# Performance work log

Measured on AMD Instinct MI355X. Metric: run time of the kernel, lower is better.

The kernel has to match this reference:

```python
import jax, jax.numpy as jnp
import numpy as np

D_MODEL = 1024
NUM_HEADS = 16
HEAD_DIM = D_MODEL // NUM_HEADS
LN_EPS = 1e-3  # keras LayerNormalization default epsilon


def setup_inputs() -> dict:
    key = jax.random.key(0)
    ks = jax.random.split(key, 10)
    B, T = 2, 2048
    s = 1.0 / np.sqrt(D_MODEL)
    return {
        "x": jax.random.normal(ks[0], (B, T, D_MODEL), dtype=jnp.float32),
        "Wq": jax.random.normal(ks[1], (D_MODEL, D_MODEL), dtype=jnp.float32) * s,
        "Wk": jax.random.normal(ks[2], (D_MODEL, D_MODEL), dtype=jnp.float32) * s,
        "Wv": jax.random.normal(ks[3], (D_MODEL, D_MODEL), dtype=jnp.float32) * s,
        "Wg": jax.random.normal(ks[4], (D_MODEL, D_MODEL), dtype=jnp.float32) * s,
        "bg": jnp.zeros((D_MODEL,), dtype=jnp.float32),
        "Wo": jax.random.normal(ks[5], (D_MODEL, D_MODEL), dtype=jnp.float32) * s,
        "bo": jnp.zeros((D_MODEL,), dtype=jnp.float32),
        "ln_gamma": jnp.ones((D_MODEL,), dtype=jnp.float32),
        "ln_beta": jnp.zeros((D_MODEL,), dtype=jnp.float32),
    }


def reference(x, Wq, Wk, Wv, Wg, bg, Wo, bo, ln_gamma, ln_beta):
    B, T, D = x.shape
    H, dh = NUM_HEADS, HEAD_DIM

    def split_heads(z):
        return z.reshape(B, T, H, dh).transpose(0, 2, 1, 3)  # [B,H,T,dh]

    Q = split_heads(x @ Wq)
    K = split_heads(x @ Wk)
    V = split_heads(x @ Wv)
    G = jax.nn.swish(x @ Wg + bg)  # [B,T,D]

    # Per-head causal decay mask D[h,m,n] = gamma_h^(m-n) for m>=n else 0
    idx = jnp.arange(T, dtype=jnp.float32)
    diff = idx[:, None] - idx[None, :]  # [T,T]
    causal = (diff >= 0).astype(jnp.float32)
    gammas = 1.0 - 2.0 ** (-5.0 - jnp.arange(H, dtype=jnp.float32))  # [H]
    Dmask = (gammas[:, None, None] ** jnp.maximum(diff, 0.0)) * causal  # [H,T,T]

    scale = float(dh) ** 0.5
    scores = jnp.einsum('bhtd,bhsd->bhts', Q, K) / scale  # [B,H,T,T]
    ret = jnp.einsum('bhts,bhsd->bhtd', scores * Dmask[None], V)  # [B,H,T,dh]
    ret = ret.transpose(0, 2, 1, 3).reshape(B, T, D)  # concat heads

    # LayerNorm (axis=-1, keras default eps=1e-3)
    mu = jnp.mean(ret, axis=-1, keepdims=True)
    var = jnp.mean(jnp.square(ret - mu), axis=-1, keepdims=True)
    ln = (ret - mu) / jnp.sqrt(var + LN_EPS) * ln_gamma + ln_beta

    return (ln * G) @ Wo + bo
```

## Files before the change

### kernel.cpp

```cpp
#include <hip/hip_runtime.h>

#define D_MODEL 1024
#define NHEADS  16
#define HDIM    64
#define BATCH   2
#define SEQ     2048
#define ROWS    (BATCH*SEQ)
#define CHUNK   128
#define NCHUNK  (SEQ/CHUNK)
#define LN_EPS  1e-3f

typedef unsigned short ushort_t;
typedef __attribute__((ext_vector_type(4))) float          f32x4;
typedef __attribute__((ext_vector_type(8))) short          s16x8;
typedef __attribute__((ext_vector_type(4))) unsigned short u16x4;
typedef __attribute__((ext_vector_type(8))) unsigned short u16x8;

__device__ __forceinline__ ushort_t f2b(float f) {
    union { float f; unsigned int u; } v; v.f = f;
    unsigned int r = v.u + 0x7fffu + ((v.u >> 16) & 1u);
    return (ushort_t)(r >> 16);
}
__device__ __forceinline__ float b2f(ushort_t b) {
    union { unsigned int u; float f; } v; v.u = ((unsigned int)b) << 16;
    return v.f;
}

__device__ __forceinline__ void async_load16(const ushort_t* g, ushort_t* l) {
    __builtin_amdgcn_global_load_lds(
        (const __attribute__((address_space(1))) unsigned int*)(g),
        (__attribute__((address_space(3))) unsigned int*)(l),
        16, 0, 0);
}

__global__ __launch_bounds__(256) void prep_kernel(
        const float* __restrict__ x,
        const float* __restrict__ Wq, const float* __restrict__ Wk,
        const float* __restrict__ Wv, const float* __restrict__ Wg,
        const float* __restrict__ Wo,
        ushort_t* __restrict__ xb, ushort_t* __restrict__ WcatT,
        ushort_t* __restrict__ WoT, float* __restrict__ rowstats) {
    __shared__ float tile[32][33];
    int bid = blockIdx.x, t = threadIdx.x;
    if (bid < 4096) {
        if (bid < 8)
            *(f32x4*)(rowstats + (bid * 256 + t) * 4) = (f32x4)0.0f;
        int idx = (bid * 256 + t) * 4;
        f32x4 v = *(const f32x4*)(x + idx);
        u16x4 o;
        o.x = f2b(v.x); o.y = f2b(v.y); o.z = f2b(v.z); o.w = f2b(v.w);
        *(u16x4*)(xb + idx) = o;
        return;
    }
    int zb = bid - 4096;
    int z = zb >> 10;
    int rem = zb & 1023;
    int bx = rem & 31, by = rem >> 5;
    const float* W = (z == 0) ? Wq : (z == 1) ? Wk : (z == 2) ? Wv : (z == 3) ? Wg : Wo;
    ushort_t* dst = (z < 4) ? (WcatT + (size_t)z * 1024 * 1024) : WoT;
    int n0 = bx * 32, k0 = by * 32;
    int tx = t & 31, ty = t >> 5;
#pragma unroll
    for (int i = 0; i < 4; i++) {
        int k = k0 + ty + i * 8;
        tile[ty + i * 8][tx] = W[(size_t)k * 1024 + n0 + tx];
    }
    __syncthreads();
#pragma unroll
    for (int i = 0; i < 4; i++) {
        int n = n0 + ty + i * 8;
        dst[(size_t)n * 1024 + k0 + tx] = f2b(tile[tx][ty + i * 8]);
    }
}

__global__ __launch_bounds__(256, 2) void gemm_kernel(
        const ushort_t* __restrict__ A, const ushort_t* __restrict__ BT,
        int K, int N, int mode, const float* __restrict__ bias,
        ushort_t* __restrict__ Yout, float* __restrict__ Fout) {
    extern __shared__ char smem[];
    ushort_t* As = (ushort_t*)smem;
    ushort_t* Bs = As + 128 * 64;
    int t = threadIdx.x;
    int row0 = blockIdx.y * 128, col0 = blockIdx.x * 128;
    int w = t >> 6, lane = t & 63;
    int wr = (w >> 1) * 64, wc = (w & 1) * 64;
    int qd = lane >> 4, ln = lane & 15;
    int lx = ln & 7;

    f32x4 acc[4][4];
#pragma unroll
    for (int i = 0; i < 4; i++)
#pragma unroll
        for (int j = 0; j < 4; j++) acc[i][j] = (f32x4)0.0f;

    for (int k0 = 0; k0 < K; k0 += 64) {
#pragma unroll
        for (int p = 0; p < 4; p++) {
            int g = p * 256 + t;
            int r = g >> 3;
            int kb = g & 7;
            int kbs = kb ^ (r & 7);
            async_load16(A + (size_t)(row0 + r) * K + k0 + kbs * 8, As + g * 8);
            async_load16(BT + (size_t)(col0 + r) * K + k0 + kbs * 8, Bs + g * 8);
        }
        __syncthreads();
#pragma unroll
        for (int kk = 0; kk < 64; kk += 32) {
            s16x8 af[4], bf[4];
            int kxa = ((kk >> 3) + qd) ^ lx;
#pragma unroll
            for (int i = 0; i < 4; i++)
                af[i] = *(const s16x8*)(As + (wr + i * 16 + ln) * 64 + kxa * 8);
#pragma unroll
            for (int j = 0; j < 4; j++)
                bf[j] = *(const s16x8*)(Bs + (wc + j * 16 + ln) * 64 + kxa * 8);
#pragma unroll
            for (int i = 0; i < 4; i++)
#pragma unroll
                for (int j = 0; j < 4; j++)
                    acc[i][j] = __builtin_amdgcn_mfma_f32_16x16x32_bf16(
                        af[i], bf[j], acc[i][j], 0, 0, 0);
        }
        __syncthreads();
    }

#pragma unroll
    for (int i = 0; i < 4; i++)
#pragma unroll
        for (int j = 0; j < 4; j++) {
            int n = col0 + wc + j * 16 + ln;
            int region = n >> 10;
#pragma unroll
            for (int r = 0; r < 4; r++) {
                int m = row0 + wr + i * 16 + qd * 4 + r;
                float v = acc[i][j][r];
                if (mode == 0) {
                    if (region == 0) v *= 0.125f;
                    else if (region == 3) {
                        v += bias[n & 1023];
                        v = v / (1.0f + __expf(-v));
                    }
                    Yout[(size_t)m * N + n] = f2b(v);
                } else {
                    Fout[(size_t)m * N + n] = v + bias[n];
                }
            }
        }
}

#define LDW 72
#define SJ 136
#define VT_LDW 136
#define CO_ELEMS (128*LDW*2 + 64*LDW*2 + 64*VT_LDW)
__global__ __launch_bounds__(256, 2) void retention_kernel(const ushort_t* __restrict__ Y,
                                                           ushort_t* __restrict__ ret,
                                                           float* __restrict__ rowstats) {
    extern __shared__ char smem[];
    ushort_t* Qs   = (ushort_t*)smem;
    ushort_t* Kc   = Qs + 128 * LDW;
    ushort_t* Sphi = Kc + 128 * LDW;
    ushort_t* Splo = Sphi + 64 * LDW;
    ushort_t* Vt   = Splo + 64 * LDW;
    ushort_t* Pl   = Qs;
    ushort_t* Ktd  = Qs;
    ushort_t* Vtd  = Ktd + 64 * SJ;

    int c_raw = blockIdx.x, h = blockIdx.y, b = blockIdx.z;
    int c = b ? (NCHUNK - 1 - c_raw) : c_raw;
    int t = threadIdx.x;
    float gamma = 1.0f - exp2f(-5.0f - (float)h);
    float l2g = log2f(gamma);
    float gC = exp2f(128.0f * l2g);
    int row0 = b * SEQ + c * CHUNK;
    int colK = D_MODEL + h * HDIM;

    int w = t >> 6, lane = t & 63;
    int wr = w * 16;
    int qd = lane >> 4, ln = lane & 15;
    int dgi = t & 7, jg = t >> 3;

    {
        u16x8 v8[4];
#pragma unroll
        for (int r = 0; r < 4; r++)
            v8[r] = *(const u16x8*)(Y + (size_t)(row0 + jg * 4 + r) * 4096
                                      + 2 * D_MODEL + h * HDIM + dgi * 8);
#pragma unroll
        for (int q = 0; q < 8; q++) {
            int qq = q ^ dgi;
            u16x4 pv;
#pragma unroll
            for (int r = 0; r < 4; r++) pv[r] = v8[r][qq];
            *(u16x4*)(Vt + (dgi * 8 + qq) * VT_LDW + jg * 4) = pv;
        }
    }

    float dec[4];
#pragma unroll
    for (int r = 0; r < 4; r++)
        dec[r] = exp2f((float)(127 - (jg * 4 + r)) * l2g);

    f32x4 Sreg[4];
#pragma unroll
    for (int nt = 0; nt < 4; nt++) Sreg[nt] = (f32x4)0.0f;

    u16x8 k8[4], v8[4];
    if (c > 0) {
        int prow0 = b * SEQ;
#pragma unroll
        for (int r = 0; r < 4; r++) {
            size_t src = (size_t)(prow0 + jg * 4 + r) * 4096 + colK + dgi * 8;
            k8[r] = *(const u16x8*)(Y + src);
            v8[r] = *(const u16x8*)(Y + src + D_MODEL);
        }
    }

    for (int cp = 0; cp < c; cp++) {
        __syncthreads();
#pragma unroll
        for (int q = 0; q < 8; q++) {
            int qq = q ^ dgi;
            u16x4 pk, pv;
#pragma unroll
            for (int r = 0; r < 4; r++) {
                pk[r] = f2b(b2f(k8[r][qq]) * dec[r]);
                pv[r] = v8[r][qq];
            }
            *(u16x4*)(Ktd + (dgi * 8 + qq) * SJ + jg * 4) = pk;
            *(u16x4*)(Vtd + (dgi * 8 + qq) * SJ + jg * 4) = pv;
        }
        __syncthreads();
        if (cp + 1 < c) {
            int prow0 = b * SEQ + (cp + 1) * CHUNK;
#pragma unroll
            for (int r = 0; r < 4; r++) {
                size_t src = (size_t)(prow0 + jg * 4 + r) * 4096 + colK + dgi * 8;
                k8[r] = *(const u16x8*)(Y + src);
                v8[r] = *(const u16x8*)(Y + src + D_MODEL);
            }
        }
        s16x8 af[4];
#pragma unroll
        for (int ks = 0; ks < 4; ks++)
            af[ks] = *(const s16x8*)(Vtd + (wr + ln) * SJ + ks * 32 + qd * 8);
#pragma unroll
        for (int nt = 0; nt < 4; nt++) {
            f32x4 a4 = (f32x4)0.0f;
#pragma unroll
            for (int ks = 0; ks < 4; ks++) {
                s16x8 bf = *(const s16x8*)(Ktd + (nt * 16 + ln) * SJ + ks * 32 + qd * 8);
                a4 = __builtin_amdgcn_mfma_f32_16x16x32_bf16(af[ks], bf, a4, 0, 0, 0);
            }
            Sreg[nt] = Sreg[nt] * gC + a4;
        }
    }
    __syncthreads();

#pragma unroll
    for (int nt = 0; nt < 4; nt++)
#pragma unroll
        for (int r = 0; r < 4; r++) {
            int d = wr + qd * 4 + r, e = nt * 16 + ln;
            float s = Sreg[nt][r];
            ushort_t hb = f2b(s);
            Sphi[d * LDW + e] = hb;
            Splo[d * LDW + e] = f2b(s - b2f(hb));
        }

    for (int g = t; g < 1024; g += 256) {
        int i = g >> 3, dg = (g & 7) * 8;
        size_t src = (size_t)(row0 + i) * 4096 + h * HDIM + dg;
        *(u16x8*)(Qs + i * LDW + dg) = *(const u16x8*)(Y + src);
        *(u16x8*)(Kc + i * LDW + dg) = *(const u16x8*)(Y + src + D_MODEL);
    }
    __syncthreads();

    int wr2 = w * 32;

    s16x8 aq[2][2];
#pragma unroll
    for (int mt = 0; mt < 2; mt++)
#pragma unroll
        for (int ks = 0; ks < 2; ks++)
            aq[mt][ks] = *(const s16x8*)(Qs + (wr2 + mt * 16 + ln) * LDW + ks * 32 + qd * 8);

    float prow[2][4], pcolm[8];
#pragma unroll
    for (int mt = 0; mt < 2; mt++)
#pragma unroll
        for (int r = 0; r < 4; r++)
            prow[mt][r] = exp2f((float)(wr2 + mt * 16 + qd * 4 + r + 1) * l2g);
#pragma unroll
    for (int nt = 0; nt < 8; nt++)
        pcolm[nt] = exp2f(-(float)(nt * 16 + ln + 1) * l2g);

    f32x4 out[2][4];
#pragma unroll
    for (int mt = 0; mt < 2; mt++)
#pragma unroll
        for (int dt = 0; dt < 4; dt++) out[mt][dt] = (f32x4)0.0f;
#pragma unroll
    for (int dt = 0; dt < 4; dt++)
#pragma unroll
        for (int ks = 0; ks < 2; ks++) {
            s16x8 bh_ = *(const s16x8*)(Sphi + (dt * 16 + ln) * LDW + ks * 32 + qd * 8);
            s16x8 bl_ = *(const s16x8*)(Splo + (dt * 16 + ln) * LDW + ks * 32 + qd * 8);
#pragma unroll
            for (int mt = 0; mt < 2; mt++) {
                out[mt][dt] = __builtin_amdgcn_mfma_f32_16x16x32_bf16(
                    aq[mt][ks], bh_, out[mt][dt], 0, 0, 0);
                out[mt][dt] = __builtin_amdgcn_mfma_f32_16x16x32_bf16(
                    aq[mt][ks], bl_, out[mt][dt], 0, 0, 0);
            }
        }
#pragma unroll
    for (int mt = 0; mt < 2; mt++)
#pragma unroll
        for (int dt = 0; dt < 4; dt++)
#pragma unroll
            for (int r = 0; r < 4; r++) out[mt][dt][r] *= prow[mt][r];

    f32x4 sc[2][8];
#pragma unroll
    for (int mt = 0; mt < 2; mt++)
#pragma unroll
        for (int nt = 0; nt < 8; nt++) sc[mt][nt] = (f32x4)0.0f;
#pragma unroll
    for (int nt = 0; nt < 8; nt++)
#pragma unroll
        for (int ks = 0; ks < 2; ks++) {
            s16x8 bk = *(const s16x8*)(Kc + (nt * 16 + ln) * LDW + ks * 32 + qd * 8);
#pragma unroll
            for (int mt = 0; mt < 2; mt++)
                sc[mt][nt] = __builtin_amdgcn_mfma_f32_16x16x32_bf16(
                    aq[mt][ks], bk, sc[mt][nt], 0, 0, 0);
        }
    __syncthreads();

#pragma unroll
    for (int mt = 0; mt < 2; mt++)
#pragma unroll
        for (int nt = 0; nt < 8; nt++) {
            int j = nt * 16 + ln;
#pragma unroll
            for (int r = 0; r < 4; r++) {
                int i = wr2 + mt * 16 + qd * 4 + r;
                float v = (j <= i) ? sc[mt][nt][r] * (prow[mt][r] * pcolm[nt]) : 0.0f;
                Pl[i * VT_LDW + j] = f2b(v);
            }
        }
    __syncthreads();

#pragma unroll
    for (int ks = 0; ks < 4; ks++) {
        s16x8 ap[2];
#pragma unroll
        for (int mt = 0; mt < 2; mt++)
            ap[mt] = *(const s16x8*)(Pl + (wr2 + mt * 16 + ln) * VT_LDW + ks * 32 + qd * 8);
#pragma unroll
        for (int dt = 0; dt < 4; dt++) {
            s16x8 bv = *(const s16x8*)(Vt + (dt * 16 + ln) * VT_LDW + ks * 32 + qd * 8);
#pragma unroll
            for (int mt = 0; mt < 2; mt++)
                out[mt][dt] = __builtin_amdgcn_mfma_f32_16x16x32_bf16(
                    ap[mt], bv, out[mt][dt], 0, 0, 0);
        }
    }

    float psum[2][4], psq[2][4];
#pragma unroll
    for (int mt = 0; mt < 2; mt++)
#pragma unroll
        for (int r = 0; r < 4; r++) { psum[mt][r] = 0.0f; psq[mt][r] = 0.0f; }
#pragma unroll
    for (int mt = 0; mt < 2; mt++)
#pragma unroll
        for (int dt = 0; dt < 4; dt++)
#pragma unroll
            for (int r = 0; r < 4; r++) {
                int i = wr2 + mt * 16 + qd * 4 + r;
                ushort_t hb = f2b(out[mt][dt][r]);
                ret[(size_t)(row0 + i) * D_MODEL + h * HDIM + dt * 16 + ln] = hb;
                float vr = b2f(hb);
                psum[mt][r] += vr;
                psq[mt][r]  += vr * vr;
            }
#pragma unroll
    for (int m = 1; m < 16; m <<= 1)
#pragma unroll
        for (int mt = 0; mt < 2; mt++)
#pragma unroll
            for (int r = 0; r < 4; r++) {
                psum[mt][r] += __shfl_xor(psum[mt][r], m);
                psq[mt][r]  += __shfl_xor(psq[mt][r], m);
            }
    if (ln == 0) {
#pragma unroll
        for (int mt = 0; mt < 2; mt++)
#pragma unroll
            for (int r = 0; r < 4; r++) {
                int i = row0 + wr2 + mt * 16 + qd * 4 + r;
                atomicAdd(rowstats + 2 * i,     psum[mt][r]);
                atomicAdd(rowstats + 2 * i + 1, psq[mt][r]);
            }
    }
}

__global__ __launch_bounds__(256) void ln_gate_kernel(const ushort_t* __restrict__ ret,
                                                      const ushort_t* __restrict__ Y,
                                                      const float* __restrict__ rowstats,
                                                      const float* __restrict__ lgam,
                                                      const float* __restrict__ lbet,
                                                      ushort_t* __restrict__ LNG) {
    int row = blockIdx.x, t = threadIdx.x;
    float s  = rowstats[2 * row];
    float sq = rowstats[2 * row + 1];
    float mu  = s * (1.0f / 1024.0f);
    float var = sq * (1.0f / 1024.0f) - mu * mu;
    float inv = rsqrtf(var + LN_EPS);
    int col = t * 4;
    u16x4 rv = *(const u16x4*)(ret + (size_t)row * D_MODEL + col);
    u16x4 ug = *(const u16x4*)(Y + (size_t)row * 4096 + 3 * D_MODEL + col);
    f32x4 ga = *(const f32x4*)(lgam + col);
    f32x4 gb = *(const f32x4*)(lbet + col);
    u16x4 o;
#pragma unroll
    for (int k = 0; k < 4; k++)
        o[k] = f2b(((b2f(rv[k]) - mu) * inv * ga[k] + gb[k]) * b2f(ug[k]));
    *(u16x4*)(LNG + (size_t)row * D_MODEL + col) = o;
}

extern "C" void kernel_launch(void* const* d_in, const int* in_sizes, int n_in,
                              void* d_out, int out_size, void* d_ws, size_t ws_size,
                              hipStream_t stream) {
    const float* x   = (const float*)d_in[0];
    const float* Wq  = (const float*)d_in[1];
    const float* Wk  = (const float*)d_in[2];
    const float* Wv  = (const float*)d_in[3];
    const float* Wg  = (const float*)d_in[4];
    const float* bg  = (const float*)d_in[5];
    const float* Wo  = (const float*)d_in[6];
    const float* bo  = (const float*)d_in[7];
    const float* lng = (const float*)d_in[8];
    const float* lnb = (const float*)d_in[9];
    float* out = (float*)d_out;

    char* ws = (char*)d_ws;
    ushort_t* xb    = (ushort_t*)(ws);
    ushort_t* WcatT = (ushort_t*)(ws + (8ull  << 20));
    ushort_t* WoT   = (ushort_t*)(ws + (16ull << 20));
    ushort_t* Yb    = (ushort_t*)(ws + (18ull << 20));
    float*    rstat = (float*)   (ws + (50ull << 20));
    ushort_t* retb  = (ushort_t*)(ws + (51ull << 20));
    ushort_t* LNGb  = (ushort_t*)(ws + (60ull << 20));

    const int GEMM_LDS = 2 * 128 * 64 * 2;
    const int CO_BYTES = CO_ELEMS * 2;

    hipFuncSetAttribute(reinterpret_cast<const void*>(gemm_kernel),
                        hipFuncAttributeMaxDynamicSharedMemorySize, GEMM_LDS);
    hipFuncSetAttribute(reinterpret_cast<const void*>(retention_kernel),
                        hipFuncAttributeMaxDynamicSharedMemorySize, CO_BYTES);

    prep_kernel<<<4096 + 5120, 256, 0, stream>>>(x, Wq, Wk, Wv, Wg, Wo,
                                                 xb, WcatT, WoT, rstat);

    gemm_kernel<<<dim3(32, 32), 256, GEMM_LDS, stream>>>(
        xb, WcatT, 1024, 4096, 0, bg, Yb, (float*)nullptr);

    retention_kernel<<<dim3(NCHUNK, NHEADS, BATCH), 256, CO_BYTES, stream>>>(
        Yb, retb, rstat);

    ln_gate_kernel<<<ROWS, 256, 0, stream>>>(retb, Yb, rstat, lng, lnb, LNGb);

    gemm_kernel<<<dim3(8, 32), 256, GEMM_LDS, stream>>>(
        LNGb, WoT, 1024, 1024, 1, bo, (ushort_t*)nullptr, out);
}
```

Before: 223.1 us.

## Precompute per-chunk KV states in separate kernel, accumulate in retention kernel

Moves the per-chunk decayed K^T V state computation into a new chunk_states_kernel that runs in parallel over all chunks and writes fp32 states to a workspace. The retention kernel then only combines prior chunk states with a decay-weighted sum read from global memory, instead of recomputing MFMAs over every prior chunk serially. This removes the O(c) serial MFMA and LDS-transpose loop and the load imbalance that the reversed-chunk ordering tried to offset. It costs an extra kernel launch and about 8MB of fp32 state traffic. The combine loop is still O(c) global reads per block.

```diff
diff --git a/kernel.cpp b/kernel.cpp
--- a/kernel.cpp
+++ b/kernel.cpp
@@ -148,11 +148,78 @@
         }
 }
 
+#define SJ 136
+__global__ __launch_bounds__(256) void chunk_states_kernel(const ushort_t* __restrict__ Y,
+                                                           float* __restrict__ Astate) {
+    __shared__ ushort_t Ktd[64 * SJ];
+    __shared__ ushort_t Vtd[64 * SJ];
+    int c = blockIdx.x, h = blockIdx.y, b = blockIdx.z;
+    int t = threadIdx.x;
+    float gamma = 1.0f - exp2f(-5.0f - (float)h);
+    float l2g = log2f(gamma);
+    int row0 = b * SEQ + c * CHUNK;
+    int colK = D_MODEL + h * HDIM;
+
+    {
+        int dgi = t & 7, jg = t >> 3;
+        u16x8 k8[4], v8[4];
+        float dec[4];
+#pragma unroll
+        for (int r = 0; r < 4; r++) {
+            int j = jg * 4 + r;
+            size_t src = (size_t)(row0 + j) * 4096 + colK + dgi * 8;
+            k8[r] = *(const u16x8*)(Y + src);
+            v8[r] = *(const u16x8*)(Y + src + D_MODEL);
+            dec[r] = exp2f((float)(127 - j) * l2g);
+        }
+#pragma unroll
+        for (int q = 0; q < 8; q++) {
+            int qq = q ^ dgi;
+            u16x4 pk, pv;
+#pragma unroll
+            for (int r = 0; r < 4; r++) {
+                pk[r] = f2b(b2f(k8[r][qq]) * dec[r]);
+                pv[r] = v8[r][qq];
+            }
+            *(u16x4*)(Ktd + (dgi * 8 + qq) * SJ + jg * 4) = pk;
+            *(u16x4*)(Vtd + (dgi * 8 + qq) * SJ + jg * 4) = pv;
+        }
+    }
+    __syncthreads();
+
+    int w = t >> 6, lane = t & 63;
+    int wr = w * 16;
+    int qd = lane >> 4, ln = lane & 15;
+
+    s16x8 af[4];
+#pragma unroll
+    for (int ks = 0; ks < 4; ks++)
+        af[ks] = *(const s16x8*)(Vtd + (wr + ln) * SJ + ks * 32 + qd * 8);
+
+    f32x4 acc[4];
+#pragma unroll
+    for (int nt = 0; nt < 4; nt++) {
+        acc[nt] = (f32x4)0.0f;
+#pragma unroll
+        for (int ks = 0; ks < 4; ks++) {
+            s16x8 bf = *(const s16x8*)(Ktd + (nt * 16 + ln) * SJ + ks * 32 + qd * 8);
+            acc[nt] = __builtin_amdgcn_mfma_f32_16x16x32_bf16(af[ks], bf, acc[nt], 0, 0, 0);
+        }
+    }
+
+    size_t base = ((size_t)((b * NHEADS + h) * NCHUNK + c)) * 4096;
+#pragma unroll
+    for (int nt = 0; nt < 4; nt++)
+#pragma unroll
+        for (int r = 0; r < 4; r++)
+            Astate[base + (size_t)(wr + qd * 4 + r) * 64 + nt * 16 + ln] = acc[nt][r];
+}
+
 #define LDW 72
-#define SJ 136
 #define VT_LDW 136
 #define CO_ELEMS (128*LDW*2 + 64*LDW*2 + 64*VT_LDW)
 __global__ __launch_bounds__(256, 2) void retention_kernel(const ushort_t* __restrict__ Y,
+                                                           const float* __restrict__ Astate,
                                                            ushort_t* __restrict__ ret,
                                                            float* __restrict__ rowstats) {
     extern __shared__ char smem[];
@@ -162,20 +229,15 @@
     ushort_t* Splo = Sphi + 64 * LDW;
     ushort_t* Vt   = Splo + 64 * LDW;
     ushort_t* Pl   = Qs;
-    ushort_t* Ktd  = Qs;
-    ushort_t* Vtd  = Ktd + 64 * SJ;
-
-    int c_raw = blockIdx.x, h = blockIdx.y, b = blockIdx.z;
-    int c = b ? (NCHUNK - 1 - c_raw) : c_raw;
+
+    int c = blockIdx.x, h = blockIdx.y, b = blockIdx.z;
     int t = threadIdx.x;
     float gamma = 1.0f - exp2f(-5.0f - (float)h);
     float l2g = log2f(gamma);
     float gC = exp2f(128.0f * l2g);
     int row0 = b * SEQ + c * CHUNK;
-    int colK = D_MODEL + h * HDIM;
 
     int w = t >> 6, lane = t & 63;
-    int wr = w * 16;
     int qd = lane >> 4, ln = lane & 15;
     int dgi = t & 7, jg = t >> 3;
 
@@ -194,84 +256,40 @@
             *(u16x4*)(Vt + (dgi * 8 + qq) * VT_LDW + jg * 4) = pv;
         }
     }
-
-    float dec[4];
-#pragma unroll
-    for (int r = 0; r < 4; r++)
-        dec[r] = exp2f((float)(127 - (jg * 4 + r)) * l2g);
-
-    f32x4 Sreg[4];
-#pragma unroll
-    for (int nt = 0; nt < 4; nt++) Sreg[nt] = (f32x4)0.0f;
-
-    u16x8 k8[4], v8[4];
-    if (c > 0) {
-        int prow0 = b * SEQ;
-#pragma unroll
-        for (int r = 0; r < 4; r++) {
-            size_t src = (size_t)(prow0 + jg * 4 + r) * 4096 + colK + dgi * 8;
-            k8[r] = *(const u16x8*)(Y + src);
-            v8[r] = *(const u16x8*)(Y + src + D_MODEL);
-        }
-    }
-
-    for (int cp = 0; cp < c; cp++) {
-        __syncthreads();
-#pragma unroll
-        for (int q = 0; q < 8; q++) {
-            int qq = q ^ dgi;
-            u16x4 pk, pv;
-#pragma unroll
-            for (int r = 0; r < 4; r++) {
-                pk[r] = f2b(b2f(k8[r][qq]) * dec[r]);
-                pv[r] = v8[r][qq];
-            }
-            *(u16x4*)(Ktd + (dgi * 8 + qq) * SJ + jg * 4) = pk;
-            *(u16x4*)(Vtd + (dgi * 8 + qq) * SJ + jg * 4) = pv;
-        }
-        __syncthreads();
-        if (cp + 1 < c) {
-            int prow0 = b * SEQ + (cp + 1) * CHUNK;
-#pragma unroll
-            for (int r = 0; r < 4; r++) {
-                size_t src = (size_t)(prow0 + jg * 4 + r) * 4096 + colK + dgi * 8;
-                k8[r] = *(const u16x8*)(Y + src);
-                v8[r] = *(const u16x8*)(Y + src + D_MODEL);
-            }
-        }
-        s16x8 af[4];
-#pragma unroll
-        for (int ks = 0; ks < 4; ks++)
-            af[ks] = *(const s16x8*)(Vtd + (wr + ln) * SJ + ks * 32 + qd * 8);
-#pragma unroll
-        for (int nt = 0; nt < 4; nt++) {
-            f32x4 a4 = (f32x4)0.0f;
-#pragma unroll
-            for (int ks = 0; ks < 4; ks++) {
-                s16x8 bf = *(const s16x8*)(Ktd + (nt * 16 + ln) * SJ + ks * 32 + qd * 8);
-                a4 = __builtin_amdgcn_mfma_f32_16x16x32_bf16(af[ks], bf, a4, 0, 0, 0);
-            }
-            Sreg[nt] = Sreg[nt] * gC + a4;
-        }
-    }
-    __syncthreads();
-
-#pragma unroll
-    for (int nt = 0; nt < 4; nt++)
-#pragma unroll
-        for (int r = 0; r < 4; r++) {
-            int d = wr + qd * 4 + r, e = nt * 16 + ln;
-            float s = Sreg[nt][r];
-            ushort_t hb = f2b(s);
-            Sphi[d * LDW + e] = hb;
-            Splo[d * LDW + e] = f2b(s - b2f(hb));
-        }
 
     for (int g = t; g < 1024; g += 256) {
         int i = g >> 3, dg = (g & 7) * 8;
         size_t src = (size_t)(row0 + i) * 4096 + h * HDIM + dg;
         *(u16x8*)(Qs + i * LDW + dg) = *(const u16x8*)(Y + src);
         *(u16x8*)(Kc + i * LDW + dg) = *(const u16x8*)(Y + src + D_MODEL);
+    }
+
+    {
+        f32x4 acc4[4];
+#pragma unroll
+        for (int k4 = 0; k4 < 4; k4++) acc4[k4] = (f32x4)0.0f;
+        size_t abase = ((size_t)((b * NHEADS + h) * NCHUNK)) * 4096 + t * 16;
+        for (int cp = 0; cp < c; cp++) {
+#pragma unroll
+            for (int k4 = 0; k4 < 4; k4++) {
+                f32x4 a = *(const f32x4*)(Astate + abase + (size_t)cp * 4096 + k4 * 4);
+                acc4[k4] = acc4[k4] * gC + a;
+            }
+        }
+        int d = t >> 2, e0 = (t & 3) * 16;
+#pragma unroll
+        for (int k4 = 0; k4 < 4; k4++) {
+            u16x4 hi4, lo4;
+#pragma unroll
+            for (int k2 = 0; k2 < 4; k2++) {
+                float s = acc4[k4][k2];
+                ushort_t hb = f2b(s);
+                hi4[k2] = hb;
+                lo4[k2] = f2b(s - b2f(hb));
+            }
+            *(u16x4*)(Sphi + d * LDW + e0 + k4 * 4) = hi4;
+            *(u16x4*)(Splo + d * LDW + e0 + k4 * 4) = lo4;
+        }
     }
     __syncthreads();
 
@@ -453,6 +471,7 @@
     float*    rstat = (float*)   (ws + (50ull << 20));
     ushort_t* retb  = (ushort_t*)(ws + (51ull << 20));
     ushort_t* LNGb  = (ushort_t*)(ws + (60ull << 20));
+    float*    Ast   = (float*)   (ws + (69ull << 20));
 
     const int GEMM_LDS = 2 * 128 * 64 * 2;
     const int CO_BYTES = CO_ELEMS * 2;
@@ -468,8 +487,10 @@
     gemm_kernel<<<dim3(32, 32), 256, GEMM_LDS, stream>>>(
         xb, WcatT, 1024, 4096, 0, bg, Yb, (float*)nullptr);
 
+    chunk_states_kernel<<<dim3(NCHUNK, NHEADS, BATCH), 256, 0, stream>>>(Yb, Ast);
+
     retention_kernel<<<dim3(NCHUNK, NHEADS, BATCH), 256, CO_BYTES, stream>>>(
-        Yb, retb, rstat);
+        Yb, Ast, retb, rstat);
 
     ln_gate_kernel<<<ROWS, 256, 0, stream>>>(retb, Yb, rstat, lng, lnb, LNGb);
 
```

New measurement: 208.1 us. 1.07x faster.
